# Kernel optimization log

Hardware: AMD Instinct MI355X
Metric: run time of the kernel (lower is better)

## Reference

```python
import jax, jax.numpy as jnp
import numpy as np

D_MODEL = 1024
N_HEADS = 16
D_K = D_MODEL // N_HEADS


def setup_inputs() -> dict:
    key = jax.random.key(0)
    ks = jax.random.split(key, 5)
    s = 1.0 / np.sqrt(D_MODEL)  # mimic Linear init scale
    x = jax.random.normal(ks[0], (4, 2048, D_MODEL), dtype=jnp.float32)
    Wq = jax.random.normal(ks[1], (D_MODEL, D_MODEL), dtype=jnp.float32) * s
    Wk = jax.random.normal(ks[2], (D_MODEL, D_MODEL), dtype=jnp.float32) * s
    Wv = jax.random.normal(ks[3], (D_MODEL, D_MODEL), dtype=jnp.float32) * s
    Wo = jax.random.normal(ks[4], (D_MODEL, D_MODEL), dtype=jnp.float32) * s
    z = jnp.zeros((D_MODEL,), dtype=jnp.float32)
    return {"x": x, "Wq": Wq, "bq": z, "Wk": Wk, "bk": z, "Wv": Wv, "bv": z, "Wo": Wo, "bo": z}


def reference(x, Wq, bq, Wk, bk, Wv, bv, Wo, bo):
    B, S, _ = x.shape
    # Linear: y = x @ W^T + b (torch convention, W is [out, in])
    def proj(W, b):
        y = jnp.einsum('bsd,ed->bse', x, W) + b
        return y.reshape(B, S, N_HEADS, D_K).transpose(0, 2, 1, 3)  # [B,H,S,Dk]
    q = proj(Wq, bq)
    k = proj(Wk, bk)
    v = proj(Wv, bv)
    scale = 1.0 / np.sqrt(D_K)
    attn = jnp.einsum('bhqd,bhkd->bhqk', q, k) * scale  # [B,H,S,S]
    attn = jax.nn.softmax(attn, axis=-1)
    out = jnp.einsum('bhqk,bhkd->bhqd', attn, v)  # [B,H,S,Dk]
    out = out.transpose(0, 2, 1, 3).reshape(B, S, D_MODEL)
    return jnp.einsum('bsd,ed->bse', out, Wo) + bo
```

## Files before the change

### kernel.cpp

```cpp
#include <hip/hip_runtime.h>
#include <hip/hip_bf16.h>
#include <stdint.h>

#define DM   1024
#define NH   16
#define DKK  64
#define BB   4
#define SSEQ 2048
#define MTOT 8192

typedef __attribute__((ext_vector_type(8))) __bf16 bf16x8;
typedef __attribute__((ext_vector_type(4))) float f32x4;
typedef __attribute__((ext_vector_type(16))) float f32x16;
typedef __attribute__((ext_vector_type(4))) unsigned int u32x4;

__device__ __forceinline__ unsigned short f2bf(float f) {
  union { float f; unsigned int u; } v; v.f = f;
  unsigned int r = v.u + 0x7FFFu + ((v.u >> 16) & 1u);
  return (unsigned short)(r >> 16);
}

__device__ __forceinline__ unsigned int cvtpk(float lo, float hi) {
  unsigned int r;
  asm("v_cvt_pk_bf16_f32 %0, %1, %2" : "=v"(r) : "v"(lo), "v"(hi));
  return r;
}

__device__ __forceinline__ void gld16(const void* g, void* l) {
  typedef __attribute__((address_space(1))) const unsigned int gq_t;
  typedef __attribute__((address_space(3))) unsigned int lq_t;
  __builtin_amdgcn_global_load_lds((gq_t*)g, (lq_t*)l, 16, 0, 0);
}

__global__ __launch_bounds__(256)
void cast5(const float* __restrict__ x,  const float* __restrict__ wq,
           const float* __restrict__ wk, const float* __restrict__ wv,
           const float* __restrict__ wo,
           unsigned short* __restrict__ xb,  unsigned short* __restrict__ wqb,
           unsigned short* __restrict__ wkb, unsigned short* __restrict__ wvb,
           unsigned short* __restrict__ wob)
{
  const int blk = blockIdx.x;
  const float* src; unsigned short* dst; int base;
  if (blk < 512) { src = x; dst = xb; base = blk * 4096; }
  else {
    const int w = (blk - 512) >> 6, i = (blk - 512) & 63;
    base = i * 4096;
    src = (w==0) ? wq : (w==1) ? wk : (w==2) ? wv : wo;
    dst = (w==0) ? wqb : (w==1) ? wkb : (w==2) ? wvb : wob;
  }
  #pragma unroll
  for (int it = 0; it < 16; ++it) {
    const int idx = base + it*256 + (int)threadIdx.x;
    const float4 v = ((const float4*)src)[idx];
    ushort4 o; o.x = f2bf(v.x); o.y = f2bf(v.y); o.z = f2bf(v.z); o.w = f2bf(v.w);
    ((ushort4*)dst)[idx] = o;
  }
}

template<int MODE>
__global__ __launch_bounds__(256, 2)
void gemm_nt(const unsigned short* __restrict__ A,
             const unsigned short* __restrict__ Bw,
             const float* __restrict__ bias,
             void* __restrict__ Cp)
{
  __shared__ unsigned short As[2][4096];
  __shared__ unsigned short Bs[2][4096];
  int wg = blockIdx.x;
  wg = (wg & 7) * 64 + (wg >> 3);
  const int bm = wg >> 3, bn = wg & 7;
  const int m0 = bm * 128, n0 = bn * 128;
  const int tid = threadIdx.x;
  const int lane = tid & 63, wv = tid >> 6;
  const int wr = wv >> 1, wc = wv & 1;
  const int lr = lane & 15, lg = lane >> 4;

  const f32x4 fz = {0.f, 0.f, 0.f, 0.f};
  f32x4 acc[4][4];
  #pragma unroll
  for (int i = 0; i < 4; ++i)
    #pragma unroll
    for (int j = 0; j < 4; ++j) acc[i][j] = fz;

  const int srow = wv*16 + (lane >> 2);
  const int scol = (lane & 3) * 8;
  const unsigned short* Abase = A  + (size_t)(m0 + srow)*DM + scol;
  const unsigned short* Bbase = Bw + (size_t)(n0 + srow)*DM + scol;

  #define GSTAGE(bufi, kt)  {                                        \
    const int kc = (kt) * 32;                                        \
    gld16(Abase + kc,          (char*)&As[bufi][0] + wv*1024);       \
    gld16(Abase + 64*DM + kc,  (char*)&As[bufi][0] + 4096 + wv*1024);\
    gld16(Bbase + kc,          (char*)&Bs[bufi][0] + wv*1024);       \
    gld16(Bbase + 64*DM + kc,  (char*)&Bs[bufi][0] + 4096 + wv*1024);}

  GSTAGE(0, 0);
  __syncthreads();

  for (int kt = 0; kt < 32; ++kt) {
    const int buf = kt & 1;
    if (kt < 31) GSTAGE(buf ^ 1, kt + 1);
    bf16x8 af[4], bf[4];
    #pragma unroll
    for (int i = 0; i < 4; ++i)
      af[i] = *(const bf16x8*)&As[buf][(wr*64 + i*16 + lr)*32 + lg*8];
    #pragma unroll
    for (int j = 0; j < 4; ++j)
      bf[j] = *(const bf16x8*)&Bs[buf][(wc*64 + j*16 + lr)*32 + lg*8];
    #pragma unroll
    for (int i = 0; i < 4; ++i)
      #pragma unroll
      for (int j = 0; j < 4; ++j)
        acc[i][j] = __builtin_amdgcn_mfma_f32_16x16x32_bf16(af[i], bf[j], acc[i][j], 0, 0, 0);
    __syncthreads();
  }
  #undef GSTAGE

  #pragma unroll
  for (int j = 0; j < 4; ++j) {
    const int n = n0 + wc*64 + j*16 + lr;
    const float bvv = bias[n];
    #pragma unroll
    for (int i = 0; i < 4; ++i) {
      #pragma unroll
      for (int r = 0; r < 4; ++r) {
        const int m = m0 + wr*64 + i*16 + lg*4 + r;
        float v = acc[i][j][r] + bvv;
        if (MODE == 3) v *= 0.18033688011112042f;
        if (MODE == 0 || MODE == 3) {
          const int b = m >> 11, s = m & 2047, h = n >> 6, d = n & 63;
          ((unsigned short*)Cp)[(size_t)((b*NH + h)*SSEQ + s)*DKK + d] = f2bf(v);
        } else if (MODE == 2) {
          const int b = m >> 11, s = m & 2047, h = n >> 6, d = n & 63;
          ((unsigned short*)Cp)[(size_t)(b*NH + h)*(SSEQ*DKK)
                                + (((s >> 4)*64 + d) << 4) + (s & 15)] = f2bf(v);
        } else {
          ((float*)Cp)[(size_t)m*DM + n] = v;
        }
      }
    }
  }
}

__device__ __forceinline__ u32x4 packP(const f32x16& sv, const int j, const int hi)
{
  const int rb = j * 8;
  const unsigned int a0 = cvtpk(sv[rb+0], sv[rb+1]);
  const unsigned int a1 = cvtpk(sv[rb+2], sv[rb+3]);
  const unsigned int b0 = cvtpk(sv[rb+4], sv[rb+5]);
  const unsigned int b1 = cvtpk(sv[rb+6], sv[rb+7]);
  const unsigned int s0_ = hi ? a0 : b0;
  const unsigned int s1_ = hi ? a1 : b1;
  const unsigned int r0 = __shfl_xor(s0_, 32, 64);
  const unsigned int r1 = __shfl_xor(s1_, 32, 64);
  u32x4 pk;
  pk[0] = hi ? r0 : a0;
  pk[1] = hi ? r1 : a1;
  pk[2] = hi ? b0 : r0;
  pk[3] = hi ? b1 : r1;
  return pk;
}

__global__ __launch_bounds__(128, 2)
void attn1d(const unsigned short* __restrict__ Q,
            const unsigned short* __restrict__ K,
            const unsigned short* __restrict__ Vp,
            unsigned short* __restrict__ AO)
{
  __shared__ unsigned short Ks[2][4096];
  const int flat = blockIdx.x;
  const int xcd = flat & 7, idx = flat >> 3;
  const int bh = xcd*8 + (idx >> 5), qt = idx & 31;
  const int b = bh >> 4, h = bh & 15;
  const int tid = threadIdx.x, lane = tid & 63, wv = tid >> 6;
  const int l31 = lane & 31, hi = lane >> 5;
  const int q0 = qt*64 + wv*32;
  const size_t hoff = (size_t)bh * SSEQ * DKK;
  const unsigned short* Qg = Q  + hoff;
  const unsigned short* Kg = K  + hoff;
  const unsigned short* Vb = Vp + hoff;

  bf16x8 qf[4];
  {
    const unsigned short* qr = Qg + (size_t)(q0 + l31)*DKK + hi*8;
    #pragma unroll
    for (int ks = 0; ks < 4; ++ks)
      qf[ks] = *(const bf16x8*)(qr + ks*16);
  }

  f32x16 oA0, oA1;
  float lacc[8];
  #pragma unroll
  for (int r = 0; r < 16; ++r) { oA0[r]=0.f; oA1[r]=0.f; }
  #pragma unroll
  for (int r = 0; r < 8; ++r) lacc[r] = 0.f;

  const int sbase = wv*4096 + lane*16;
  const int cbyte = hi * 16;

  #define STAGE(bufi, kv0)                                                        \
    _Pragma("unroll")                                                             \
    for (int it = 0; it < 4; ++it) {                                              \
      const int LB  = sbase + it*1024;                                            \
      const int row = LB >> 7;                                                    \
      const int cb  = (LB & 127) ^ ((row & 7) << 4);                              \
      gld16(Kg + (size_t)((kv0) + row)*DKK + (cb >> 1),                           \
            (char*)&Ks[bufi][0] + LB);                                            \
    }

  STAGE(0, 0);
  __syncthreads();

  for (int kv = 0; kv < 32; ++kv) {
    const int buf = kv & 1;
    const int kv0 = kv * 64;
    if (kv < 31) { STAGE(buf ^ 1, kv0 + 64); }
    const char* KsB = (const char*)&Ks[buf][0];
    const unsigned short* vbase = Vb + (kv0 >> 4)*1024 + l31*16 + hi*8;

    #pragma unroll
    for (int hf = 0; hf < 2; ++hf) {
      bf16x8 vf0[2], vf1[2];
      #pragma unroll
      for (int j = 0; j < 2; ++j) {
        vf0[j] = *(const bf16x8*)(vbase + (2*hf + j)*1024);
        vf1[j] = *(const bf16x8*)(vbase + (2*hf + j)*1024 + 512);
      }

      f32x16 s;
      #pragma unroll
      for (int r = 0; r < 16; ++r) s[r] = 0.f;
      __builtin_amdgcn_s_setprio(1);
      #pragma unroll
      for (int ks = 0; ks < 4; ++ks) {
        const int bo = l31*128 + ((ks*32 + cbyte) ^ ((l31 & 7) << 4));
        const bf16x8 kf = *(const bf16x8*)(KsB + hf*4096 + bo);
        s = __builtin_amdgcn_mfma_f32_32x32x16_bf16(kf, qf[ks], s, 0, 0, 0);
      }
      __builtin_amdgcn_s_setprio(0);

      #pragma unroll
      for (int r = 0; r < 16; ++r) {
        s[r] = __builtin_amdgcn_exp2f(s[r]);
        lacc[r & 7] += s[r];
      }

      __builtin_amdgcn_s_setprio(1);
      #pragma unroll
      for (int j = 0; j < 2; ++j) {
        const u32x4 pk = packP(s, j, hi);
        const bf16x8 pb = __builtin_bit_cast(bf16x8, pk);
        oA0 = __builtin_amdgcn_mfma_f32_32x32x16_bf16(vf0[j], pb, oA0, 0, 0, 0);
        oA1 = __builtin_amdgcn_mfma_f32_32x32x16_bf16(vf1[j], pb, oA1, 0, 0, 0);
      }
      __builtin_amdgcn_s_setprio(0);
    }
    __syncthreads();
  }

  float lA = ((lacc[0]+lacc[1])+(lacc[2]+lacc[3]))
           + ((lacc[4]+lacc[5])+(lacc[6]+lacc[7]));
  lA += __shfl_xor(lA, 32, 64);
  const float inv = 1.f / lA;

  char* lds = (char*)&Ks[0][0] + wv*4096;
  {
    const int row = l31;
    const int swz = (l31 & 7) << 4;
    #pragma unroll
    for (int db = 0; db < 2; ++db) {
      const f32x16& o = db ? oA1 : oA0;
      #pragma unroll
      for (int r = 0; r < 16; r += 2) {
        const int d = db*32 + (r & 3) + 8*(r >> 2) + 4*hi;
        *(unsigned int*)(lds + row*128 + ((d*2) ^ swz)) = cvtpk(o[r]*inv, o[r+1]*inv);
      }
    }
  }
  __syncthreads();
  {
    const int q = q0 + l31;
    unsigned short* orow = AO + (size_t)(b*SSEQ + q)*DM + h*DKK;
    const int swz = (l31 & 7) << 4;
    #pragma unroll
    for (int it = 0; it < 4; ++it) {
      const int c16 = hi + 2*it;
      const uint4 v = *(const uint4*)(lds + l31*128 + ((c16*16) ^ swz));
      *(uint4*)(orow + c16*8) = v;
    }
  }
  #undef STAGE
}

extern "C" void kernel_launch(void* const* d_in, const int* in_sizes, int n_in,
                              void* d_out, int out_size, void* d_ws, size_t ws_size,
                              hipStream_t stream)
{
  (void)in_sizes; (void)n_in; (void)out_size; (void)ws_size;
  const float* x  = (const float*)d_in[0];
  const float* Wq = (const float*)d_in[1];
  const float* bq = (const float*)d_in[2];
  const float* Wk = (const float*)d_in[3];
  const float* bk = (const float*)d_in[4];
  const float* Wv = (const float*)d_in[5];
  const float* bv = (const float*)d_in[6];
  const float* Wo = (const float*)d_in[7];
  const float* bo = (const float*)d_in[8];

  char* ws = (char*)d_ws;
  unsigned short* xb  = (unsigned short*)(ws + 0);
  unsigned short* wqb = (unsigned short*)(ws + 16777216);
  unsigned short* wkb = (unsigned short*)(ws + 18874368);
  unsigned short* wvb = (unsigned short*)(ws + 20971520);
  unsigned short* wob = (unsigned short*)(ws + 23068672);
  unsigned short* Qb  = (unsigned short*)(ws + 25165824);
  unsigned short* Kb  = (unsigned short*)(ws + 41943040);
  unsigned short* Vpb = (unsigned short*)(ws + 58720256);
  unsigned short* AO  = xb;

  cast5<<<768, 256, 0, stream>>>(x, Wq, Wk, Wv, Wo, xb, wqb, wkb, wvb, wob);
  gemm_nt<3><<<512, 256, 0, stream>>>(xb, wqb, bq, Qb);
  gemm_nt<0><<<512, 256, 0, stream>>>(xb, wkb, bk, Kb);
  gemm_nt<2><<<512, 256, 0, stream>>>(xb, wvb, bv, Vpb);
  attn1d<<<2048, 128, 0, stream>>>(Qb, Kb, Vpb, AO);
  gemm_nt<1><<<512, 256, 0, stream>>>(AO, wob, bo, (float*)d_out);
}
```

Baseline: 212.4 us.

## Deepen GEMM K-tile with swizzled LDS; make attention single-wave blocks without barriers

The projection GEMM now stages 64-wide K tiles into larger, XOR-swizzled LDS buffers and runs half as many outer iterations, which cuts barrier count and LDS bank conflicts. The attention kernel becomes one wave per block over 32-query tiles with 32-key steps. It drops __syncthreads in favour of explicit vmcnt/lgkmcnt waits, with a peeled last iteration. This aims to remove intra-block sync stalls and raise occupancy, at the cost of less K-tile reuse across waves and more global K loads.

```diff
diff --git a/kernel.cpp b/kernel.cpp
--- a/kernel.cpp
+++ b/kernel.cpp
@@ -65,8 +65,8 @@
              const float* __restrict__ bias,
              void* __restrict__ Cp)
 {
-  __shared__ unsigned short As[2][4096];
-  __shared__ unsigned short Bs[2][4096];
+  __shared__ unsigned short As[2][8192];
+  __shared__ unsigned short Bs[2][8192];
   int wg = blockIdx.x;
   wg = (wg & 7) * 64 + (wg >> 3);
   const int bm = wg >> 3, bn = wg & 7;
@@ -83,36 +83,48 @@
     #pragma unroll
     for (int j = 0; j < 4; ++j) acc[i][j] = fz;
 
-  const int srow = wv*16 + (lane >> 2);
-  const int scol = (lane & 3) * 8;
-  const unsigned short* Abase = A  + (size_t)(m0 + srow)*DM + scol;
-  const unsigned short* Bbase = Bw + (size_t)(n0 + srow)*DM + scol;
-
-  #define GSTAGE(bufi, kt)  {                                        \
-    const int kc = (kt) * 32;                                        \
-    gld16(Abase + kc,          (char*)&As[bufi][0] + wv*1024);       \
-    gld16(Abase + 64*DM + kc,  (char*)&As[bufi][0] + 4096 + wv*1024);\
-    gld16(Bbase + kc,          (char*)&Bs[bufi][0] + wv*1024);       \
-    gld16(Bbase + 64*DM + kc,  (char*)&Bs[bufi][0] + 4096 + wv*1024);}
+  const int srow = wv*32 + (lane >> 3);
+  const int scolb = ((lane & 7) * 16) ^ ((lane >> 3) << 4);
+  const unsigned short* Abase = A  + (size_t)(m0 + srow)*DM + (scolb >> 1);
+  const unsigned short* Bbase = Bw + (size_t)(n0 + srow)*DM + (scolb >> 1);
+
+  #define GSTAGE(bufi, kt)  {                                               \
+    const int kc = (kt) * 64;                                               \
+    _Pragma("unroll")                                                       \
+    for (int c = 0; c < 4; ++c) {                                           \
+      gld16(Abase + (size_t)c*8*DM + kc,                                    \
+            (char*)&As[bufi][0] + wv*4096 + c*1024);                        \
+      gld16(Bbase + (size_t)c*8*DM + kc,                                    \
+            (char*)&Bs[bufi][0] + wv*4096 + c*1024);                        \
+    } }
 
   GSTAGE(0, 0);
   __syncthreads();
 
-  for (int kt = 0; kt < 32; ++kt) {
+  for (int kt = 0; kt < 16; ++kt) {
     const int buf = kt & 1;
-    if (kt < 31) GSTAGE(buf ^ 1, kt + 1);
-    bf16x8 af[4], bf[4];
-    #pragma unroll
-    for (int i = 0; i < 4; ++i)
-      af[i] = *(const bf16x8*)&As[buf][(wr*64 + i*16 + lr)*32 + lg*8];
-    #pragma unroll
-    for (int j = 0; j < 4; ++j)
-      bf[j] = *(const bf16x8*)&Bs[buf][(wc*64 + j*16 + lr)*32 + lg*8];
-    #pragma unroll
-    for (int i = 0; i < 4; ++i)
-      #pragma unroll
-      for (int j = 0; j < 4; ++j)
-        acc[i][j] = __builtin_amdgcn_mfma_f32_16x16x32_bf16(af[i], bf[j], acc[i][j], 0, 0, 0);
+    if (kt < 15) GSTAGE(buf ^ 1, kt + 1);
+    #pragma unroll
+    for (int kk = 0; kk < 2; ++kk) {
+      bf16x8 af[4], bf[4];
+      #pragma unroll
+      for (int i = 0; i < 4; ++i) {
+        const int row = wr*64 + i*16 + lr;
+        af[i] = *(const bf16x8*)((char*)&As[buf][0] + row*128
+                 + ((kk*64 + lg*16) ^ ((lr & 7) << 4)));
+      }
+      #pragma unroll
+      for (int j = 0; j < 4; ++j) {
+        const int row = wc*64 + j*16 + lr;
+        bf[j] = *(const bf16x8*)((char*)&Bs[buf][0] + row*128
+                 + ((kk*64 + lg*16) ^ ((lr & 7) << 4)));
+      }
+      #pragma unroll
+      for (int i = 0; i < 4; ++i)
+        #pragma unroll
+        for (int j = 0; j < 4; ++j)
+          acc[i][j] = __builtin_amdgcn_mfma_f32_16x16x32_bf16(af[i], bf[j], acc[i][j], 0, 0, 0);
+    }
     __syncthreads();
   }
   #undef GSTAGE
@@ -162,20 +174,20 @@
   return pk;
 }
 
-__global__ __launch_bounds__(128, 2)
-void attn1d(const unsigned short* __restrict__ Q,
+__global__ __launch_bounds__(64, 4)
+void attn1w(const unsigned short* __restrict__ Q,
             const unsigned short* __restrict__ K,
             const unsigned short* __restrict__ Vp,
             unsigned short* __restrict__ AO)
 {
-  __shared__ unsigned short Ks[2][4096];
+  __shared__ unsigned short Ks[2][2048];
   const int flat = blockIdx.x;
   const int xcd = flat & 7, idx = flat >> 3;
-  const int bh = xcd*8 + (idx >> 5), qt = idx & 31;
+  const int bh = xcd*8 + (idx >> 6), qt = idx & 63;
   const int b = bh >> 4, h = bh & 15;
-  const int tid = threadIdx.x, lane = tid & 63, wv = tid >> 6;
+  const int lane = (int)threadIdx.x & 63;
   const int l31 = lane & 31, hi = lane >> 5;
-  const int q0 = qt*64 + wv*32;
+  const int q0 = qt * 32;
   const size_t hoff = (size_t)bh * SSEQ * DKK;
   const unsigned short* Qg = Q  + hoff;
   const unsigned short* Kg = K  + hoff;
@@ -196,13 +208,10 @@
   #pragma unroll
   for (int r = 0; r < 8; ++r) lacc[r] = 0.f;
 
-  const int sbase = wv*4096 + lane*16;
-  const int cbyte = hi * 16;
-
   #define STAGE(bufi, kv0)                                                        \
     _Pragma("unroll")                                                             \
     for (int it = 0; it < 4; ++it) {                                              \
-      const int LB  = sbase + it*1024;                                            \
+      const int LB  = lane*16 + it*1024;                                          \
       const int row = LB >> 7;                                                    \
       const int cb  = (LB & 127) ^ ((row & 7) << 4);                              \
       gld16(Kg + (size_t)((kv0) + row)*DKK + (cb >> 1),                           \
@@ -210,23 +219,22 @@
     }
 
   STAGE(0, 0);
-  __syncthreads();
-
-  for (int kv = 0; kv < 32; ++kv) {
+
+  for (int kv = 0; kv < 64; ++kv) {
     const int buf = kv & 1;
-    const int kv0 = kv * 64;
-    if (kv < 31) { STAGE(buf ^ 1, kv0 + 64); }
-    const char* KsB = (const char*)&Ks[buf][0];
-    const unsigned short* vbase = Vb + (kv0 >> 4)*1024 + l31*16 + hi*8;
-
-    #pragma unroll
-    for (int hf = 0; hf < 2; ++hf) {
+    const int kv0 = kv * 32;
+
+    if (kv < 63) {
+      STAGE(buf ^ 1, kv0 + 32);
+      const unsigned short* vbase = Vb + (size_t)(kv*2)*1024 + l31*16 + hi*8;
       bf16x8 vf0[2], vf1[2];
       #pragma unroll
       for (int j = 0; j < 2; ++j) {
-        vf0[j] = *(const bf16x8*)(vbase + (2*hf + j)*1024);
-        vf1[j] = *(const bf16x8*)(vbase + (2*hf + j)*1024 + 512);
-      }
+        vf0[j] = *(const bf16x8*)(vbase + j*1024);
+        vf1[j] = *(const bf16x8*)(vbase + j*1024 + 512);
+      }
+      asm volatile("s_waitcnt vmcnt(8)" ::: "memory");
+      __builtin_amdgcn_sched_barrier(0);
 
       f32x16 s;
       #pragma unroll
@@ -234,8 +242,8 @@
       __builtin_amdgcn_s_setprio(1);
       #pragma unroll
       for (int ks = 0; ks < 4; ++ks) {
-        const int bo = l31*128 + ((ks*32 + cbyte) ^ ((l31 & 7) << 4));
-        const bf16x8 kf = *(const bf16x8*)(KsB + hf*4096 + bo);
+        const int bo = l31*128 + ((ks*32 + hi*16) ^ ((l31 & 7) << 4));
+        const bf16x8 kf = *(const bf16x8*)((const char*)&Ks[buf][0] + bo);
         s = __builtin_amdgcn_mfma_f32_32x32x16_bf16(kf, qf[ks], s, 0, 0, 0);
       }
       __builtin_amdgcn_s_setprio(0);
@@ -255,8 +263,39 @@
         oA1 = __builtin_amdgcn_mfma_f32_32x32x16_bf16(vf1[j], pb, oA1, 0, 0, 0);
       }
       __builtin_amdgcn_s_setprio(0);
-    }
-    __syncthreads();
+    } else {
+      const unsigned short* vbase = Vb + (size_t)(kv*2)*1024 + l31*16 + hi*8;
+      bf16x8 vf0[2], vf1[2];
+      #pragma unroll
+      for (int j = 0; j < 2; ++j) {
+        vf0[j] = *(const bf16x8*)(vbase + j*1024);
+        vf1[j] = *(const bf16x8*)(vbase + j*1024 + 512);
+      }
+      asm volatile("s_waitcnt vmcnt(4)" ::: "memory");
+      __builtin_amdgcn_sched_barrier(0);
+
+      f32x16 s;
+      #pragma unroll
+      for (int r = 0; r < 16; ++r) s[r] = 0.f;
+      #pragma unroll
+      for (int ks = 0; ks < 4; ++ks) {
+        const int bo = l31*128 + ((ks*32 + hi*16) ^ ((l31 & 7) << 4));
+        const bf16x8 kf = *(const bf16x8*)((const char*)&Ks[buf][0] + bo);
+        s = __builtin_amdgcn_mfma_f32_32x32x16_bf16(kf, qf[ks], s, 0, 0, 0);
+      }
+      #pragma unroll
+      for (int r = 0; r < 16; ++r) {
+        s[r] = __builtin_amdgcn_exp2f(s[r]);
+        lacc[r & 7] += s[r];
+      }
+      #pragma unroll
+      for (int j = 0; j < 2; ++j) {
+        const u32x4 pk = packP(s, j, hi);
+        const bf16x8 pb = __builtin_bit_cast(bf16x8, pk);
+        oA0 = __builtin_amdgcn_mfma_f32_32x32x16_bf16(vf0[j], pb, oA0, 0, 0, 0);
+        oA1 = __builtin_amdgcn_mfma_f32_32x32x16_bf16(vf1[j], pb, oA1, 0, 0, 0);
+      }
+    }
   }
 
   float lA = ((lacc[0]+lacc[1])+(lacc[2]+lacc[3]))
@@ -264,7 +303,7 @@
   lA += __shfl_xor(lA, 32, 64);
   const float inv = 1.f / lA;
 
-  char* lds = (char*)&Ks[0][0] + wv*4096;
+  char* lds = (char*)&Ks[0][0];
   {
     const int row = l31;
     const int swz = (l31 & 7) << 4;
@@ -278,10 +317,10 @@
       }
     }
   }
-  __syncthreads();
+  asm volatile("s_waitcnt lgkmcnt(0)" ::: "memory");
+  __builtin_amdgcn_sched_barrier(0);
   {
-    const int q = q0 + l31;
-    unsigned short* orow = AO + (size_t)(b*SSEQ + q)*DM + h*DKK;
+    unsigned short* orow = AO + (size_t)(b*SSEQ + q0 + l31)*DM + h*DKK;
     const int swz = (l31 & 7) << 4;
     #pragma unroll
     for (int it = 0; it < 4; ++it) {
@@ -323,6 +362,6 @@
   gemm_nt<3><<<512, 256, 0, stream>>>(xb, wqb, bq, Qb);
   gemm_nt<0><<<512, 256, 0, stream>>>(xb, wkb, bk, Kb);
   gemm_nt<2><<<512, 256, 0, stream>>>(xb, wvb, bv, Vpb);
-  attn1d<<<2048, 128, 0, stream>>>(Qb, Kb, Vpb, AO);
+  attn1w<<<4096, 64, 0, stream>>>(Qb, Kb, Vpb, AO);
   gemm_nt<1><<<512, 256, 0, stream>>>(AO, wob, bo, (float*)d_out);
 }
```

New measurement: 201.9 us. 5.0% less time.

## Double GEMM K-tile to 64 and XOR-swizzle shared memory layout

Applied to the files above, without the earlier changes.

The projection GEMM now stages a K-chunk of 64 instead of 32 per iteration, which halves the loop trip count and the number of block barriers. Shared memory rows are stored with an XOR swizzle on the 16-byte column chunk to avoid LDS bank conflicts on the fragment reads. LDS use doubles to 64KB per block, which may reduce occupancy at two blocks per CU.

```diff
diff --git a/kernel.cpp b/kernel.cpp
--- a/kernel.cpp
+++ b/kernel.cpp
@@ -65,8 +65,8 @@
              const float* __restrict__ bias,
              void* __restrict__ Cp)
 {
-  __shared__ unsigned short As[2][4096];
-  __shared__ unsigned short Bs[2][4096];
+  __shared__ unsigned short As[2][8192];
+  __shared__ unsigned short Bs[2][8192];
   int wg = blockIdx.x;
   wg = (wg & 7) * 64 + (wg >> 3);
   const int bm = wg >> 3, bn = wg & 7;
@@ -83,36 +83,48 @@
     #pragma unroll
     for (int j = 0; j < 4; ++j) acc[i][j] = fz;
 
-  const int srow = wv*16 + (lane >> 2);
-  const int scol = (lane & 3) * 8;
-  const unsigned short* Abase = A  + (size_t)(m0 + srow)*DM + scol;
-  const unsigned short* Bbase = Bw + (size_t)(n0 + srow)*DM + scol;
-
-  #define GSTAGE(bufi, kt)  {                                        \
-    const int kc = (kt) * 32;                                        \
-    gld16(Abase + kc,          (char*)&As[bufi][0] + wv*1024);       \
-    gld16(Abase + 64*DM + kc,  (char*)&As[bufi][0] + 4096 + wv*1024);\
-    gld16(Bbase + kc,          (char*)&Bs[bufi][0] + wv*1024);       \
-    gld16(Bbase + 64*DM + kc,  (char*)&Bs[bufi][0] + 4096 + wv*1024);}
+  const int srow = wv*32 + (lane >> 3);
+  const int scolb = ((lane & 7) * 16) ^ ((lane >> 3) << 4);
+  const unsigned short* Abase = A  + (size_t)(m0 + srow)*DM + (scolb >> 1);
+  const unsigned short* Bbase = Bw + (size_t)(n0 + srow)*DM + (scolb >> 1);
+
+  #define GSTAGE(bufi, kt)  {                                               \
+    const int kc = (kt) * 64;                                               \
+    _Pragma("unroll")                                                       \
+    for (int c = 0; c < 4; ++c) {                                           \
+      gld16(Abase + (size_t)c*8*DM + kc,                                    \
+            (char*)&As[bufi][0] + wv*4096 + c*1024);                        \
+      gld16(Bbase + (size_t)c*8*DM + kc,                                    \
+            (char*)&Bs[bufi][0] + wv*4096 + c*1024);                        \
+    } }
 
   GSTAGE(0, 0);
   __syncthreads();
 
-  for (int kt = 0; kt < 32; ++kt) {
+  for (int kt = 0; kt < 16; ++kt) {
     const int buf = kt & 1;
-    if (kt < 31) GSTAGE(buf ^ 1, kt + 1);
-    bf16x8 af[4], bf[4];
-    #pragma unroll
-    for (int i = 0; i < 4; ++i)
-      af[i] = *(const bf16x8*)&As[buf][(wr*64 + i*16 + lr)*32 + lg*8];
-    #pragma unroll
-    for (int j = 0; j < 4; ++j)
-      bf[j] = *(const bf16x8*)&Bs[buf][(wc*64 + j*16 + lr)*32 + lg*8];
-    #pragma unroll
-    for (int i = 0; i < 4; ++i)
-      #pragma unroll
-      for (int j = 0; j < 4; ++j)
-        acc[i][j] = __builtin_amdgcn_mfma_f32_16x16x32_bf16(af[i], bf[j], acc[i][j], 0, 0, 0);
+    if (kt < 15) GSTAGE(buf ^ 1, kt + 1);
+    #pragma unroll
+    for (int kk = 0; kk < 2; ++kk) {
+      bf16x8 af[4], bf[4];
+      #pragma unroll
+      for (int i = 0; i < 4; ++i) {
+        const int row = wr*64 + i*16 + lr;
+        af[i] = *(const bf16x8*)((char*)&As[buf][0] + row*128
+                 + ((kk*64 + lg*16) ^ ((lr & 7) << 4)));
+      }
+      #pragma unroll
+      for (int j = 0; j < 4; ++j) {
+        const int row = wc*64 + j*16 + lr;
+        bf[j] = *(const bf16x8*)((char*)&Bs[buf][0] + row*128
+                 + ((kk*64 + lg*16) ^ ((lr & 7) << 4)));
+      }
+      #pragma unroll
+      for (int i = 0; i < 4; ++i)
+        #pragma unroll
+        for (int j = 0; j < 4; ++j)
+          acc[i][j] = __builtin_amdgcn_mfma_f32_16x16x32_bf16(af[i], bf[j], acc[i][j], 0, 0, 0);
+    }
     __syncthreads();
   }
   #undef GSTAGE
```

Measured after the change: 194.1 us (median of 2 runs). 8.6% less time.
